# Performance work log

Hardware: AMD Instinct MI355X
Metric: run time of the kernel (lower is better)

The kernel has to match this reference:

```python
import jax, jax.numpy as jnp
import numpy as np

N = 100000   # nodes
E = 300000   # edges per snapshot
S = 5        # snapshots
D_IN = 128   # node_dim
H = 256      # hidden dim
P = 10000    # post nodes


def setup_inputs() -> dict:
    key = jax.random.key(0)
    ks = jax.random.split(key, 8)
    node_features = jax.random.normal(ks[0], (N, D_IN), jnp.float32)
    edge_index = jax.random.randint(ks[1], (S, 2, E), 0, N, dtype=jnp.int64)
    post_idx = jax.random.randint(ks[2], (P,), 0, N, dtype=jnp.int64)
    glorot = lambda k, sh, fan: jax.random.normal(k, sh, jnp.float32) * (1.0 / np.sqrt(fan))
    return {
        'node_features': node_features,
        'edge_index': edge_index,
        'post_idx': post_idx,
        'W1': glorot(ks[3], (D_IN, H), D_IN), 'b1': jnp.zeros((H,), jnp.float32),
        'W2': glorot(ks[4], (H, H), H),       'b2': jnp.zeros((H,), jnp.float32),
        'Wc1': glorot(ks[5], (H, H // 2), H), 'bc1': jnp.zeros((H // 2,), jnp.float32),
        'Wc2': glorot(ks[6], (H // 2, 1), H // 2), 'bc2': jnp.zeros((1,), jnp.float32),
    }


def gcn_conv(x, src, dst, W, b):
    """PyG GCNConv: h = D^-1/2 (A+I) D^-1/2 (x W) + b, aggregate at target (dst)."""
    n = x.shape[0]
    h = x @ W                                   # [n, out]
    loop = jnp.arange(n, dtype=src.dtype)
    src2 = jnp.concatenate([src, loop])          # add self-loops
    dst2 = jnp.concatenate([dst, loop])
    deg = jax.ops.segment_sum(jnp.ones_like(dst2, jnp.float32), dst2, num_segments=n)
    dinv = jnp.where(deg > 0, jax.lax.rsqrt(deg), 0.0)
    norm = dinv[src2] * dinv[dst2]               # [E+n]
    out = jax.ops.segment_sum(h[src2] * norm[:, None], dst2, num_segments=n)
    return out + b


def reference(node_features, edge_index, post_idx, W1, b1, W2, b2, Wc1, bc1, Wc2, bc2):
    embs = []
    for s in range(edge_index.shape[0]):  # loop over fixed small snapshot count
        src, dst = edge_index[s, 0], edge_index[s, 1]
        # layer 0: 128 -> 256, relu, no skip (dims differ)
        x1 = jax.nn.relu(gcn_conv(node_features, src, dst, W1, b1))
        # layer 1 (last): 256 -> 256, no relu, residual skip
        x2 = gcn_conv(x1, src, dst, W2, b2) + x1
        embs.append(x2)
    agg = jnp.mean(jnp.stack(embs, axis=0), axis=0)  # mean over snapshots
    post = agg[post_idx]                             # [P, H]
    logits = jax.nn.relu(post @ Wc1 + bc1) @ Wc2 + bc2
    return jax.nn.sigmoid(logits[:, 0])              # [P]
```

## Files before the change

kernel.cpp:

```cpp
#include <hip/hip_runtime.h>
#include <hip/hip_bf16.h>
#include <math.h>

#define NN 100000
#define NE 300000
#define NS 5
#define DIN 128
#define HID 256
#define NP 10000
#define NB_N 391

#define NBUCK 1024
#define NBUCK_USED 782
#define PBLK 64
#define EPB 19
#define BCAP 2048
#define CAPR 40960
#define NCPAD 16
#define LDB 136
#define LDO 260

typedef short s8v __attribute__((ext_vector_type(8)));
typedef float f4v __attribute__((ext_vector_type(4)));

static __device__ __forceinline__ float bf2f(unsigned short u) {
    union { unsigned int i; float f; } v; v.i = ((unsigned int)u) << 16; return v.f;
}
static __device__ __forceinline__ unsigned short f2bf(float f) {
    union { float f; unsigned int i; } v; v.f = f;
    return (unsigned short)((v.i + 0x7fff + ((v.i >> 16) & 1)) >> 16);
}


__global__ void setpost_kernel(const int* __restrict__ post, int* __restrict__ isPost,
                               int* __restrict__ needed) {
    int i = blockIdx.x * 256 + threadIdx.x;
    int s = blockIdx.y;
    if (i < NP) {
        int nd = post[i];
        needed[(size_t)s * NN + nd] = 1;
        if (s == 0) isPost[nd] = 1;
    }
}


__global__ void hist_kernel(const int* __restrict__ EI, int* __restrict__ bhist) {
    __shared__ int h[NBUCK];
    int s = blockIdx.y, b = blockIdx.x, t = threadIdx.x;
    for (int q = t; q < NBUCK; q += 256) h[q] = 0;
    __syncthreads();
    const int* dstp = EI + (size_t)s * 2 * NE + NE;
    int e0 = b * (EPB * 256);
    #pragma unroll
    for (int j = 0; j < EPB; j++) {
        int e = e0 + j * 256 + t;
        if (e < NE) atomicAdd(&h[dstp[e] >> 7], 1);
    }
    __syncthreads();
    for (int q = t; q < NBUCK; q += 256)
        if (h[q]) atomicAdd(&bhist[s * NBUCK + q], h[q]);
}

__global__ void bscan_kernel(const int* __restrict__ bhist, int* __restrict__ bbase,
                             int* __restrict__ bcur) {
    __shared__ int sm[NBUCK];
    int s = blockIdx.x, t = threadIdx.x;
    int v = bhist[s * NBUCK + t];
    sm[t] = v;
    __syncthreads();
    for (int d = 1; d < NBUCK; d <<= 1) {
        int x = (t >= d) ? sm[t - d] : 0;
        __syncthreads();
        sm[t] += x;
        __syncthreads();
    }
    int base = sm[t] - v;
    bbase[s * NBUCK + t] = base;
    bcur[s * NBUCK + t] = base;
}

__global__ void part_kernel(const int* __restrict__ EI, int* __restrict__ bcur,
                            int2* __restrict__ pairs) {
    __shared__ int h[NBUCK];
    __shared__ int base[NBUCK];
    int s = blockIdx.y, b = blockIdx.x, t = threadIdx.x;
    for (int q = t; q < NBUCK; q += 256) h[q] = 0;
    __syncthreads();
    const int* srcp = EI + (size_t)s * 2 * NE;
    const int* dstp = srcp + NE;
    int e0 = b * (EPB * 256);
    int rs[EPB], rd[EPB];
    #pragma unroll
    for (int j = 0; j < EPB; j++) {
        int e = e0 + j * 256 + t;
        if (e < NE) {
            rs[j] = srcp[e];
            rd[j] = dstp[e];
            atomicAdd(&h[rd[j] >> 7], 1);
        } else {
            rd[j] = -1; rs[j] = 0;
        }
    }
    __syncthreads();
    for (int q = t; q < NBUCK; q += 256) {
        int c = h[q];
        base[q] = c ? atomicAdd(&bcur[s * NBUCK + q], c) : 0;
    }
    __syncthreads();
    #pragma unroll
    for (int j = 0; j < EPB; j++) {
        if (rd[j] >= 0) {
            int pos = atomicAdd(&base[rd[j] >> 7], 1);
            pairs[(size_t)s * NE + pos] = make_int2(rs[j], rd[j]);
        }
    }
}

__global__ void bucket_csr_kernel(const int2* __restrict__ pairs, const int* __restrict__ bbase,
                                  const int* __restrict__ bhist, const int* __restrict__ isPost,
                                  int* __restrict__ cnt, int* __restrict__ offs,
                                  float* __restrict__ dinv, int* __restrict__ csr,
                                  int* __restrict__ needed) {
    __shared__ int nh[128];
    __shared__ int noff[128];
    __shared__ int sbuf[BCAP];
    int s = blockIdx.y, b = blockIdx.x, t = threadIdx.x;
    int base = bbase[s * NBUCK + b];
    int count = bhist[s * NBUCK + b];
    if (count > BCAP) count = BCAP;
    if (t < 128) nh[t] = 0;
    __syncthreads();
    const int2* pp = pairs + (size_t)s * NE + base;
    for (int e = t; e < count; e += 256)
        atomicAdd(&nh[pp[e].y & 127], 1);
    __syncthreads();
    if (t < 128) noff[t] = nh[t];
    __syncthreads();
    for (int d = 1; d < 128; d <<= 1) {
        int x = 0;
        if (t < 128 && t >= d) x = noff[t - d];
        __syncthreads();
        if (t < 128) noff[t] += x;
        __syncthreads();
    }
    if (t < 128) {
        int excl = noff[t] - nh[t];
        noff[t] = excl;
        int g = b * 128 + t;
        if (g < NN) {
            int c = nh[t];
            cnt[(size_t)s * NN + g]  = c;
            offs[(size_t)s * NN + g] = base + excl;
            dinv[(size_t)s * NN + g] = rsqrtf((float)(c + 1));
        }
    }
    __syncthreads();
    for (int e = t; e < count; e += 256) {
        int2 pr = pp[e];
        int pos = atomicAdd(&noff[pr.y & 127], 1);
        sbuf[pos] = pr.x;
        if (isPost[pr.y]) needed[(size_t)s * NN + pr.x] = 1;
    }
    __syncthreads();
    for (int e = t; e < count; e += 256)
        csr[(size_t)s * NE + base + e] = sbuf[e];
}


__global__ void compact_kernel(const int* __restrict__ needed, int* __restrict__ ncount,
                               int* __restrict__ list, int* __restrict__ inv) {
    __shared__ int wcnt[4];
    __shared__ int gbase;
    int s = blockIdx.y;
    int i = blockIdx.x * 256 + threadIdx.x;
    int wave = threadIdx.x >> 6, lane = threadIdx.x & 63;
    bool pred = (i < NN) && (needed[(size_t)s * NN + i] != 0);
    unsigned long long mask = __ballot(pred);
    int wc = __popcll(mask);
    if (lane == 0) wcnt[wave] = wc;
    __syncthreads();
    if (threadIdx.x == 0) {
        int tot = wcnt[0] + wcnt[1] + wcnt[2] + wcnt[3];
        gbase = tot ? atomicAdd(&ncount[s * NCPAD], tot) : 0;
    }
    __syncthreads();
    if (pred) {
        int wbase = gbase;
        #pragma unroll
        for (int q = 0; q < 4; q++) if (q < wave) wbase += wcnt[q];
        int rank = __popcll(mask & ((1ull << lane) - 1ull));
        int slot = wbase + rank;
        if (slot < CAPR) {
            list[(size_t)s * NN + slot] = i;
            inv[(size_t)s * NN + i] = slot;
        }
    }
}


__global__ void cvt_kernel(const float* __restrict__ src, unsigned short* __restrict__ dstp, int n4) {
    int i = blockIdx.x * 256 + threadIdx.x;
    if (i < n4) {
        float4 v = *(const float4*)&src[(size_t)i * 4];
        ushort4 o;
        o.x = f2bf(v.x); o.y = f2bf(v.y); o.z = f2bf(v.z); o.w = f2bf(v.w);
        *(ushort4*)&dstp[(size_t)i * 4] = o;
    }
}

__global__ void tw_kernel(const float* __restrict__ W, unsigned short* __restrict__ Wt,
                          int K, int Ncols) {
    int i = blockIdx.x * 256 + threadIdx.x;
    if (i < K * Ncols) {
        int n = i / K, k = i - n * K;
        Wt[i] = f2bf(W[(size_t)k * Ncols + n]);
    }
}


__global__ __launch_bounds__(512) void agg_mm1_kernel(
        const unsigned short* __restrict__ Xb, const unsigned short* __restrict__ W1t,
        const int* __restrict__ ncount, const float* __restrict__ dinvA,
        const int* __restrict__ offsA, const int* __restrict__ cntA,
        const int* __restrict__ csrA, const int* __restrict__ listA,
        const float* __restrict__ b1, unsigned short* __restrict__ x1cA) {
    int s = blockIdx.y;
    int M = ncount[s * NCPAD];
    if (M > CAPR) M = CAPR;
    if (blockIdx.x * 128 >= M) return;
    const float* dinv = dinvA + (size_t)s * NN;
    const int* offs = offsA + (size_t)s * NN;
    const int* cnt  = cntA + (size_t)s * NN;
    const int* csr  = csrA + (size_t)s * NE;
    const int* list = listA + (size_t)s * NN;
    unsigned short* x1c = x1cA + (size_t)s * CAPR * HID;

    __shared__ unsigned short ldsbuf[256 * LDB];
    int tid = threadIdx.x;
    for (int q = tid; q < 256 * 16; q += 512) {
        int n = q >> 4;
        int k8 = (q & 15) * 8;
        *(s8v*)&ldsbuf[n * LDB + k8] = *(const s8v*)&W1t[n * 128 + k8];
    }
    __syncthreads();

    int wave = tid >> 6, lane = tid & 63, lr = lane & 15, g = lane >> 4;
    int rowbase = blockIdx.x * 128 + wave * 16;
    int arow = rowbase + lr;

    float ga[4][8];
    #pragma unroll
    for (int kk = 0; kk < 4; kk++)
        #pragma unroll
        for (int j = 0; j < 8; j++) ga[kk][j] = 0.f;
    float di = 0.f;

    if (arow < M) {
        int node = list[arow];
        int o = offs[node], c = cnt[node];
        di = dinv[node];
        const unsigned short* rp = Xb + (size_t)node * DIN + g * 8;
        #pragma unroll
        for (int kk = 0; kk < 4; kk++) {
            s8v h = *(const s8v*)(rp + kk * 32);
            #pragma unroll
            for (int j = 0; j < 8; j++) ga[kk][j] = di * bf2f((unsigned short)h[j]);
        }
        for (int k = 0; k < c; k++) {
            int sv = csr[o + k];
            float wgt = dinv[sv];
            const unsigned short* sp = Xb + (size_t)sv * DIN + g * 8;
            #pragma unroll
            for (int kk = 0; kk < 4; kk++) {
                s8v h = *(const s8v*)(sp + kk * 32);
                #pragma unroll
                for (int j = 0; j < 8; j++) ga[kk][j] += wgt * bf2f((unsigned short)h[j]);
            }
        }
    }

    f4v acc[16];
    #pragma unroll
    for (int t8 = 0; t8 < 16; t8++) acc[t8] = (f4v){0.f, 0.f, 0.f, 0.f};
    #pragma unroll
    for (int kk = 0; kk < 4; kk++) {
        s8v a;
        #pragma unroll
        for (int j = 0; j < 8; j++) a[j] = (short)f2bf(ga[kk][j]);
        #pragma unroll
        for (int t8 = 0; t8 < 16; t8++) {
            s8v b = *(const s8v*)&ldsbuf[(t8 * 16 + lr) * LDB + kk * 32 + g * 8];
            acc[t8] = __builtin_amdgcn_mfma_f32_16x16x32_bf16(a, b, acc[t8], 0, 0, 0);
        }
    }

    __syncthreads();

    #pragma unroll
    for (int r = 0; r < 4; r++) {
        int lrow = wave * 16 + g * 4 + r;
        float sc = __shfl(di, g * 4 + r, 64);
        #pragma unroll
        for (int t8 = 0; t8 < 16; t8++) {
            int col = t8 * 16 + lr;
            float v = sc * acc[t8][r] + b1[col];
            ldsbuf[lrow * LDO + col] = f2bf(v > 0.f ? v : 0.f);
        }
    }
    __syncthreads();

    int nrows = M - blockIdx.x * 128;
    if (nrows > 128) nrows = 128;
    for (int q = tid; q < 128 * 32; q += 512) {
        int row = q >> 5;
        if (row < nrows) {
            int c8 = (q & 31) * 8;
            *(s8v*)&x1c[(size_t)(blockIdx.x * 128 + row) * HID + c8] =
                *(const s8v*)&ldsbuf[row * LDO + c8];
        }
    }
}


__global__ void z2_kernel(const unsigned short* __restrict__ x1cA, const float* __restrict__ dinvA,
                          const int* __restrict__ offsA, const int* __restrict__ cntA,
                          const int* __restrict__ csrA, const int* __restrict__ invA,
                          const int* __restrict__ post, unsigned short* __restrict__ z2bA) {
    int s = blockIdx.y;
    const unsigned short* x1c = x1cA + (size_t)s * CAPR * HID;
    const float* dinv = dinvA + (size_t)s * NN;
    const int* offs = offsA + (size_t)s * NN;
    const int* cnt  = cntA + (size_t)s * NN;
    const int* csr  = csrA + (size_t)s * NE;
    const int* inv  = invA + (size_t)s * NN;
    unsigned short* z2b = z2bA + (size_t)s * NP * HID;

    int wave = threadIdx.x >> 6, lane = threadIdx.x & 63;
    int eg = lane >> 4, el = lane & 15;
    int p = blockIdx.x * 4 + wave;
    if (p >= NP) return;
    int node = post[p];
    int o = offs[node], c = cnt[node];
    float acc0[8] = {0.f, 0.f, 0.f, 0.f, 0.f, 0.f, 0.f, 0.f};
    float acc1[8] = {0.f, 0.f, 0.f, 0.f, 0.f, 0.f, 0.f, 0.f};
    for (int k = eg; k < c; k += 4) {
        int sv = csr[o + k];
        float wgt = dinv[sv];
        int r = inv[sv];
        const unsigned short* rp = &x1c[(size_t)r * HID + el * 16];
        s8v h0 = *(const s8v*)rp;
        s8v h1 = *(const s8v*)(rp + 8);
        #pragma unroll
        for (int j = 0; j < 8; j++) {
            acc0[j] += wgt * bf2f((unsigned short)h0[j]);
            acc1[j] += wgt * bf2f((unsigned short)h1[j]);
        }
    }
    if (eg == 0) {
        float di = dinv[node];
        int r = inv[node];
        const unsigned short* rp = &x1c[(size_t)r * HID + el * 16];
        s8v h0 = *(const s8v*)rp;
        s8v h1 = *(const s8v*)(rp + 8);
        #pragma unroll
        for (int j = 0; j < 8; j++) {
            acc0[j] += di * bf2f((unsigned short)h0[j]);
            acc1[j] += di * bf2f((unsigned short)h1[j]);
        }
    }
    #pragma unroll
    for (int j = 0; j < 8; j++) {
        acc0[j] += __shfl_xor(acc0[j], 16, 64);
        acc0[j] += __shfl_xor(acc0[j], 32, 64);
        acc1[j] += __shfl_xor(acc1[j], 16, 64);
        acc1[j] += __shfl_xor(acc1[j], 32, 64);
    }
    if (eg == 0) {
        s8v o0, o1;
        #pragma unroll
        for (int j = 0; j < 8; j++) {
            o0[j] = (short)f2bf(acc0[j]);
            o1[j] = (short)f2bf(acc1[j]);
        }
        unsigned short* wp = &z2b[(size_t)p * HID + el * 16];
        *(s8v*)wp = o0;
        *(s8v*)(wp + 8) = o1;
    }
}


__global__ __launch_bounds__(512) void mm2_kernel(
        const unsigned short* __restrict__ z2bA,
        const unsigned short* __restrict__ W2t,
        const float* __restrict__ dinvA,
        const int* __restrict__ post,
        const int* __restrict__ invA,
        const float* __restrict__ b2,
        const unsigned short* __restrict__ x1cA,
        float* __restrict__ aggPA) {
    int s = blockIdx.z;
    const unsigned short* A = z2bA + (size_t)s * NP * HID;
    const float* dinv = dinvA + (size_t)s * NN;
    const int* inv = invA + (size_t)s * NN;
    const unsigned short* x1c = x1cA + (size_t)s * CAPR * HID;
    float* Out = aggPA + (size_t)s * NP * HID;

    __shared__ unsigned short lds[128 * (HID + 8)];
    int tid = threadIdx.x;
    int colbase = blockIdx.y * 128;
    for (int q = tid; q < 128 * 32; q += 512) {
        int n = q >> 5;
        int k8 = (q & 31) * 8;
        *(s8v*)&lds[n * (HID + 8) + k8] = *(const s8v*)&W2t[(size_t)(colbase + n) * HID + k8];
    }
    __syncthreads();

    int wave = tid >> 6, lane = tid & 63, lr = lane & 15, g = lane >> 4;
    int rowbase = blockIdx.x * 128 + wave * 16;
    int arow = rowbase + lr;

    f4v acc[8];
    #pragma unroll
    for (int t = 0; t < 8; t++) acc[t] = (f4v){0.f, 0.f, 0.f, 0.f};

    #pragma unroll
    for (int kk = 0; kk < HID / 32; kk++) {
        s8v a = (s8v){0, 0, 0, 0, 0, 0, 0, 0};
        if (arow < NP) a = *(const s8v*)&A[(size_t)arow * HID + kk * 32 + g * 8];
        #pragma unroll
        for (int t = 0; t < 8; t++) {
            s8v b = *(const s8v*)&lds[(t * 16 + lr) * (HID + 8) + kk * 32 + g * 8];
            acc[t] = __builtin_amdgcn_mfma_f32_16x16x32_bf16(a, b, acc[t], 0, 0, 0);
        }
    }

    int orow0 = rowbase + g * 4;
    #pragma unroll
    for (int r = 0; r < 4; r++) {
        int row = orow0 + r;
        if (row < NP) {
            int nd = post[row];
            float sc = dinv[nd];
            size_t x1row = (size_t)inv[nd] * HID;
            #pragma unroll
            for (int t = 0; t < 8; t++) {
                int col = colbase + t * 16 + lr;
                Out[(size_t)row * HID + col] =
                    sc * acc[t][r] + b2[col] + bf2f(x1c[x1row + col]);
            }
        }
    }
}


__global__ void redcvt_kernel(const float* __restrict__ aggPA, unsigned short* __restrict__ aggPb) {
    int i = blockIdx.x * 256 + threadIdx.x;
    if (i < NP * HID / 4) {
        float4 a = *(const float4*)&aggPA[(size_t)i * 4];
        #pragma unroll
        for (int s = 1; s < NS; s++) {
            float4 b = *(const float4*)&aggPA[(size_t)s * NP * HID + (size_t)i * 4];
            a.x += b.x; a.y += b.y; a.z += b.z; a.w += b.w;
        }
        ushort4 o;
        o.x = f2bf(a.x); o.y = f2bf(a.y); o.z = f2bf(a.z); o.w = f2bf(a.w);
        *(ushort4*)&aggPb[(size_t)i * 4] = o;
    }
}


__global__ void mm3_kernel(const unsigned short* __restrict__ A,
                           const unsigned short* __restrict__ Bt,
                           const float* __restrict__ bias,
                           float* __restrict__ Out) {
    int tid = threadIdx.x;
    int wave = tid >> 6, lane = tid & 63, lr = lane & 15, g = lane >> 4;
    int rowbase = blockIdx.x * 64 + wave * 16;
    int arow = rowbase + lr;

    f4v acc[8];
    #pragma unroll
    for (int t = 0; t < 8; t++) acc[t] = (f4v){0.f, 0.f, 0.f, 0.f};

    #pragma unroll
    for (int kk = 0; kk < HID / 32; kk++) {
        s8v a = (s8v){0, 0, 0, 0, 0, 0, 0, 0};
        if (arow < NP) a = *(const s8v*)&A[(size_t)arow * HID + kk * 32 + g * 8];
        #pragma unroll
        for (int t = 0; t < 8; t++) {
            s8v b = *(const s8v*)&Bt[(size_t)(t * 16 + lr) * HID + kk * 32 + g * 8];
            acc[t] = __builtin_amdgcn_mfma_f32_16x16x32_bf16(a, b, acc[t], 0, 0, 0);
        }
    }

    int orow0 = rowbase + g * 4;
    #pragma unroll
    for (int r = 0; r < 4; r++) {
        int row = orow0 + r;
        if (row < NP) {
            #pragma unroll
            for (int t = 0; t < 8; t++) {
                int col = t * 16 + lr;
                float v = 0.2f * acc[t][r] + bias[col];
                Out[(size_t)row * 128 + col] = v > 0.f ? v : 0.f;
            }
        }
    }
}

__global__ void final_kernel(const float* __restrict__ hid, const float* __restrict__ Wc2,
                             const float* __restrict__ bc2, float* __restrict__ out) {
    int wave = threadIdx.x >> 6;
    int lane = threadIdx.x & 63;
    int p = blockIdx.x * 4 + wave;
    if (p >= NP) return;
    float part = hid[(size_t)p * 128 + lane] * Wc2[lane]
               + hid[(size_t)p * 128 + 64 + lane] * Wc2[64 + lane];
    for (int off = 32; off; off >>= 1) part += __shfl_down(part, off, 64);
    if (lane == 0) out[p] = 1.f / (1.f + expf(-(part + bc2[0])));
}


extern "C" void kernel_launch(void* const* d_in, const int* in_sizes, int n_in,
                              void* d_out, int out_size, void* d_ws, size_t ws_size,
                              hipStream_t stream) {
    const float* X    = (const float*)d_in[0];
    const int*   EI   = (const int*)d_in[1];
    const int*   post = (const int*)d_in[2];
    const float* W1   = (const float*)d_in[3];
    const float* b1   = (const float*)d_in[4];
    const float* W2   = (const float*)d_in[5];
    const float* b2   = (const float*)d_in[6];
    const float* Wc1  = (const float*)d_in[7];
    const float* bc1  = (const float*)d_in[8];
    const float* Wc2  = (const float*)d_in[9];
    const float* bc2  = (const float*)d_in[10];
    float* out = (float*)d_out;

    char* w = (char*)d_ws;
    auto carve = [&](size_t bytes) {
        void* p = (void*)w;
        w += (bytes + 255) & ~(size_t)255;
        return p;
    };
    unsigned short* Xb    = (unsigned short*)carve((size_t)NN * DIN * 2);
    unsigned short* x1c   = (unsigned short*)carve((size_t)NS * CAPR * HID * 2);
    unsigned short* z2b5  = (unsigned short*)carve((size_t)NS * NP * HID * 2);
    float* aggP5          = (float*)carve((size_t)NS * NP * HID * 4);
    unsigned short* aggPb = (unsigned short*)carve((size_t)NP * HID * 2);
    float* hid            = (float*)carve((size_t)NP * 128 * 4);
    unsigned short* W1t   = (unsigned short*)carve((size_t)256 * 128 * 2);
    unsigned short* W2t   = (unsigned short*)carve((size_t)256 * 256 * 2);
    unsigned short* Wc1t  = (unsigned short*)carve((size_t)128 * 256 * 2);
    float* dinv           = (float*)carve((size_t)NS * NN * 4);
    int*   cnt            = (int*)carve((size_t)NS * NN * 4);
    int*   offs           = (int*)carve((size_t)NS * NN * 4);
    int*   needed         = (int*)carve((size_t)NS * NN * 4);
    int*   list           = (int*)carve((size_t)NS * NN * 4);
    int*   inv            = (int*)carve((size_t)NS * NN * 4);
    int*   isPost         = (int*)carve((size_t)NN * 4);
    int*   bhist          = (int*)carve((size_t)NS * NBUCK * 4);
    int*   bbase          = (int*)carve((size_t)NS * NBUCK * 4);
    int*   bcur           = (int*)carve((size_t)NS * NBUCK * 4);
    int*   ncount         = (int*)carve((size_t)NS * NCPAD * 4);
    int*   csr            = (int*)carve((size_t)NS * NE * 4);
    int2*  pairs          = (int2*)x1c;

    hipMemsetAsync(needed, 0, (size_t)NS * NN * 4, stream);
    hipMemsetAsync(isPost, 0, (size_t)NN * 4, stream);
    hipMemsetAsync(bhist, 0, (size_t)NS * NBUCK * 4, stream);
    hipMemsetAsync(ncount, 0, (size_t)NS * NCPAD * 4, stream);

    cvt_kernel<<<(NN * DIN / 4 + 255) / 256, 256, 0, stream>>>(X, Xb, NN * DIN / 4);
    tw_kernel<<<(128 * 256 + 255) / 256, 256, 0, stream>>>(W1, W1t, 128, 256);
    tw_kernel<<<(256 * 256 + 255) / 256, 256, 0, stream>>>(W2, W2t, 256, 256);
    tw_kernel<<<(256 * 128 + 255) / 256, 256, 0, stream>>>(Wc1, Wc1t, 256, 128);
    setpost_kernel<<<dim3((NP + 255) / 256, NS), 256, 0, stream>>>(post, isPost, needed);

    hist_kernel<<<dim3(PBLK, NS), 256, 0, stream>>>(EI, bhist);
    bscan_kernel<<<NS, NBUCK, 0, stream>>>(bhist, bbase, bcur);
    part_kernel<<<dim3(PBLK, NS), 256, 0, stream>>>(EI, bcur, pairs);
    bucket_csr_kernel<<<dim3(NBUCK_USED, NS), 256, 0, stream>>>(pairs, bbase, bhist, isPost,
                                                                cnt, offs, dinv, csr, needed);
    compact_kernel<<<dim3(NB_N, NS), 256, 0, stream>>>(needed, ncount, list, inv);

    agg_mm1_kernel<<<dim3((CAPR + 127) / 128, NS), 512, 0, stream>>>(
        Xb, W1t, ncount, dinv, offs, cnt, csr, list, b1, x1c);
    z2_kernel<<<dim3((NP + 3) / 4, NS), 256, 0, stream>>>(
        x1c, dinv, offs, cnt, csr, inv, post, z2b5);
    mm2_kernel<<<dim3((NP + 127) / 128, 2, NS), 512, 0, stream>>>(
        z2b5, W2t, dinv, post, inv, b2, x1c, aggP5);

    redcvt_kernel<<<(NP * HID / 4 + 255) / 256, 256, 0, stream>>>(aggP5, aggPb);
    mm3_kernel<<<(NP + 63) / 64, 256, 0, stream>>>(aggPb, Wc1t, bc1, hid);
    final_kernel<<<(NP + 3) / 4, 256, 0, stream>>>(hid, Wc2, bc2, out);
}
```

Baseline: 244.8 us.

## Fuse snapshot reduction into mm2, fuse classifier head, merge prep kernels

mm2 now loops over all five snapshots inside one block and accumulates the epilogue in registers, writing the bf16 snapshot-sum directly. This removes the fp32 per-snapshot aggP buffer and the separate redcvt pass. mm3 and the final dot/sigmoid are fused through an LDS tile, and the four weight/feature conversion kernels are merged into one launch. The trade-off is a smaller mm2 grid with each block doing five times the work, which cuts parallelism.

```diff
diff --git a/kernel.cpp b/kernel.cpp
--- a/kernel.cpp
+++ b/kernel.cpp
@@ -40,6 +40,33 @@
         int nd = post[i];
         needed[(size_t)s * NN + nd] = 1;
         if (s == 0) isPost[nd] = 1;
+    }
+}
+
+
+__global__ void prep_kernel(const float* __restrict__ X, unsigned short* __restrict__ Xb,
+                            const float* __restrict__ W1, unsigned short* __restrict__ W1t,
+                            const float* __restrict__ W2, unsigned short* __restrict__ W2t,
+                            const float* __restrict__ Wc1, unsigned short* __restrict__ Wc1t) {
+    int b = blockIdx.x, t = threadIdx.x;
+    if (b < 12500) {
+        int i = b * 256 + t;
+        float4 v = *(const float4*)&X[(size_t)i * 4];
+        ushort4 o;
+        o.x = f2bf(v.x); o.y = f2bf(v.y); o.z = f2bf(v.z); o.w = f2bf(v.w);
+        *(ushort4*)&Xb[(size_t)i * 4] = o;
+    } else if (b < 12628) {
+        int i = (b - 12500) * 256 + t;
+        int n = i >> 7, k = i & 127;
+        W1t[i] = f2bf(W1[(size_t)k * 256 + n]);
+    } else if (b < 12884) {
+        int i = (b - 12628) * 256 + t;
+        int n = i >> 8, k = i & 255;
+        W2t[i] = f2bf(W2[(size_t)k * 256 + n]);
+    } else {
+        int i = (b - 12884) * 256 + t;
+        int n = i >> 8, k = i & 255;
+        Wc1t[i] = f2bf(Wc1[(size_t)k * 128 + n]);
     }
 }
 
@@ -194,26 +221,6 @@
             list[(size_t)s * NN + slot] = i;
             inv[(size_t)s * NN + i] = slot;
         }
-    }
-}
-
-
-__global__ void cvt_kernel(const float* __restrict__ src, unsigned short* __restrict__ dstp, int n4) {
-    int i = blockIdx.x * 256 + threadIdx.x;
-    if (i < n4) {
-        float4 v = *(const float4*)&src[(size_t)i * 4];
-        ushort4 o;
-        o.x = f2bf(v.x); o.y = f2bf(v.y); o.z = f2bf(v.z); o.w = f2bf(v.w);
-        *(ushort4*)&dstp[(size_t)i * 4] = o;
-    }
-}
-
-__global__ void tw_kernel(const float* __restrict__ W, unsigned short* __restrict__ Wt,
-                          int K, int Ncols) {
-    int i = blockIdx.x * 256 + threadIdx.x;
-    if (i < K * Ncols) {
-        int n = i / K, k = i - n * K;
-        Wt[i] = f2bf(W[(size_t)k * Ncols + n]);
     }
 }
 
@@ -389,7 +396,7 @@
 }
 
 
-__global__ __launch_bounds__(512) void mm2_kernel(
+__global__ __launch_bounds__(256) void mm2_kernel(
         const unsigned short* __restrict__ z2bA,
         const unsigned short* __restrict__ W2t,
         const float* __restrict__ dinvA,
@@ -397,18 +404,11 @@
         const int* __restrict__ invA,
         const float* __restrict__ b2,
         const unsigned short* __restrict__ x1cA,
-        float* __restrict__ aggPA) {
-    int s = blockIdx.z;
-    const unsigned short* A = z2bA + (size_t)s * NP * HID;
-    const float* dinv = dinvA + (size_t)s * NN;
-    const int* inv = invA + (size_t)s * NN;
-    const unsigned short* x1c = x1cA + (size_t)s * CAPR * HID;
-    float* Out = aggPA + (size_t)s * NP * HID;
-
+        unsigned short* __restrict__ aggPb) {
     __shared__ unsigned short lds[128 * (HID + 8)];
     int tid = threadIdx.x;
     int colbase = blockIdx.y * 128;
-    for (int q = tid; q < 128 * 32; q += 512) {
+    for (int q = tid; q < 128 * 32; q += 256) {
         int n = q >> 5;
         int k8 = (q & 31) * 8;
         *(s8v*)&lds[n * (HID + 8) + k8] = *(const s8v*)&W2t[(size_t)(colbase + n) * HID + k8];
@@ -416,108 +416,113 @@
     __syncthreads();
 
     int wave = tid >> 6, lane = tid & 63, lr = lane & 15, g = lane >> 4;
-    int rowbase = blockIdx.x * 128 + wave * 16;
+    int rowbase = blockIdx.x * 64 + wave * 16;
     int arow = rowbase + lr;
-
-    f4v acc[8];
-    #pragma unroll
-    for (int t = 0; t < 8; t++) acc[t] = (f4v){0.f, 0.f, 0.f, 0.f};
-
-    #pragma unroll
-    for (int kk = 0; kk < HID / 32; kk++) {
-        s8v a = (s8v){0, 0, 0, 0, 0, 0, 0, 0};
-        if (arow < NP) a = *(const s8v*)&A[(size_t)arow * HID + kk * 32 + g * 8];
-        #pragma unroll
-        for (int t = 0; t < 8; t++) {
-            s8v b = *(const s8v*)&lds[(t * 16 + lr) * (HID + 8) + kk * 32 + g * 8];
-            acc[t] = __builtin_amdgcn_mfma_f32_16x16x32_bf16(a, b, acc[t], 0, 0, 0);
-        }
-    }
-
     int orow0 = rowbase + g * 4;
-    #pragma unroll
-    for (int r = 0; r < 4; r++) {
-        int row = orow0 + r;
-        if (row < NP) {
-            int nd = post[row];
-            float sc = dinv[nd];
-            size_t x1row = (size_t)inv[nd] * HID;
+
+    f4v epi[8];
+    #pragma unroll
+    for (int t = 0; t < 8; t++) epi[t] = (f4v){0.f, 0.f, 0.f, 0.f};
+
+    for (int s = 0; s < NS; s++) {
+        const unsigned short* A = z2bA + (size_t)s * NP * HID;
+        const float* dinv = dinvA + (size_t)s * NN;
+        const int* inv = invA + (size_t)s * NN;
+        const unsigned short* x1c = x1cA + (size_t)s * CAPR * HID;
+
+        f4v acc[8];
+        #pragma unroll
+        for (int t = 0; t < 8; t++) acc[t] = (f4v){0.f, 0.f, 0.f, 0.f};
+        #pragma unroll
+        for (int kk = 0; kk < HID / 32; kk++) {
+            s8v a = (s8v){0, 0, 0, 0, 0, 0, 0, 0};
+            if (arow < NP) a = *(const s8v*)&A[(size_t)arow * HID + kk * 32 + g * 8];
             #pragma unroll
             for (int t = 0; t < 8; t++) {
-                int col = colbase + t * 16 + lr;
-                Out[(size_t)row * HID + col] =
-                    sc * acc[t][r] + b2[col] + bf2f(x1c[x1row + col]);
+                s8v b = *(const s8v*)&lds[(t * 16 + lr) * (HID + 8) + kk * 32 + g * 8];
+                acc[t] = __builtin_amdgcn_mfma_f32_16x16x32_bf16(a, b, acc[t], 0, 0, 0);
             }
         }
-    }
-}
-
-
-__global__ void redcvt_kernel(const float* __restrict__ aggPA, unsigned short* __restrict__ aggPb) {
-    int i = blockIdx.x * 256 + threadIdx.x;
-    if (i < NP * HID / 4) {
-        float4 a = *(const float4*)&aggPA[(size_t)i * 4];
-        #pragma unroll
-        for (int s = 1; s < NS; s++) {
-            float4 b = *(const float4*)&aggPA[(size_t)s * NP * HID + (size_t)i * 4];
-            a.x += b.x; a.y += b.y; a.z += b.z; a.w += b.w;
-        }
-        ushort4 o;
-        o.x = f2bf(a.x); o.y = f2bf(a.y); o.z = f2bf(a.z); o.w = f2bf(a.w);
-        *(ushort4*)&aggPb[(size_t)i * 4] = o;
-    }
-}
-
-
-__global__ void mm3_kernel(const unsigned short* __restrict__ A,
-                           const unsigned short* __restrict__ Bt,
-                           const float* __restrict__ bias,
-                           float* __restrict__ Out) {
-    int tid = threadIdx.x;
-    int wave = tid >> 6, lane = tid & 63, lr = lane & 15, g = lane >> 4;
-    int rowbase = blockIdx.x * 64 + wave * 16;
-    int arow = rowbase + lr;
-
-    f4v acc[8];
-    #pragma unroll
-    for (int t = 0; t < 8; t++) acc[t] = (f4v){0.f, 0.f, 0.f, 0.f};
-
-    #pragma unroll
-    for (int kk = 0; kk < HID / 32; kk++) {
-        s8v a = (s8v){0, 0, 0, 0, 0, 0, 0, 0};
-        if (arow < NP) a = *(const s8v*)&A[(size_t)arow * HID + kk * 32 + g * 8];
-        #pragma unroll
-        for (int t = 0; t < 8; t++) {
-            s8v b = *(const s8v*)&Bt[(size_t)(t * 16 + lr) * HID + kk * 32 + g * 8];
-            acc[t] = __builtin_amdgcn_mfma_f32_16x16x32_bf16(a, b, acc[t], 0, 0, 0);
-        }
-    }
-
-    int orow0 = rowbase + g * 4;
+        #pragma unroll
+        for (int r = 0; r < 4; r++) {
+            int row = orow0 + r;
+            if (row < NP) {
+                int nd = post[row];
+                float sc = dinv[nd];
+                size_t x1row = (size_t)inv[nd] * HID;
+                #pragma unroll
+                for (int t = 0; t < 8; t++) {
+                    int col = colbase + t * 16 + lr;
+                    epi[t][r] += sc * acc[t][r] + bf2f(x1c[x1row + col]);
+                }
+            }
+        }
+    }
+
     #pragma unroll
     for (int r = 0; r < 4; r++) {
         int row = orow0 + r;
         if (row < NP) {
             #pragma unroll
             for (int t = 0; t < 8; t++) {
-                int col = t * 16 + lr;
-                float v = 0.2f * acc[t][r] + bias[col];
-                Out[(size_t)row * 128 + col] = v > 0.f ? v : 0.f;
+                int col = colbase + t * 16 + lr;
+                aggPb[(size_t)row * HID + col] = f2bf(epi[t][r] + (float)NS * b2[col]);
             }
         }
     }
 }
 
-__global__ void final_kernel(const float* __restrict__ hid, const float* __restrict__ Wc2,
-                             const float* __restrict__ bc2, float* __restrict__ out) {
-    int wave = threadIdx.x >> 6;
-    int lane = threadIdx.x & 63;
-    int p = blockIdx.x * 4 + wave;
-    if (p >= NP) return;
-    float part = hid[(size_t)p * 128 + lane] * Wc2[lane]
-               + hid[(size_t)p * 128 + 64 + lane] * Wc2[64 + lane];
-    for (int off = 32; off; off >>= 1) part += __shfl_down(part, off, 64);
-    if (lane == 0) out[p] = 1.f / (1.f + expf(-(part + bc2[0])));
+
+__global__ __launch_bounds__(256) void mm3f_kernel(
+        const unsigned short* __restrict__ A, const unsigned short* __restrict__ Bt,
+        const float* __restrict__ bc1, const float* __restrict__ Wc2,
+        const float* __restrict__ bc2, float* __restrict__ out) {
+    __shared__ float tile[64 * 133];
+    __shared__ float wc2s[128];
+    int tid = threadIdx.x;
+    if (tid < 128) wc2s[tid] = Wc2[tid];
+    int wave = tid >> 6, lane = tid & 63, lr = lane & 15, g = lane >> 4;
+    int rowbase = blockIdx.x * 64 + wave * 16;
+    int arow = rowbase + lr;
+
+    f4v acc[8];
+    #pragma unroll
+    for (int t = 0; t < 8; t++) acc[t] = (f4v){0.f, 0.f, 0.f, 0.f};
+
+    #pragma unroll
+    for (int kk = 0; kk < HID / 32; kk++) {
+        s8v a = (s8v){0, 0, 0, 0, 0, 0, 0, 0};
+        if (arow < NP) a = *(const s8v*)&A[(size_t)arow * HID + kk * 32 + g * 8];
+        #pragma unroll
+        for (int t = 0; t < 8; t++) {
+            s8v b = *(const s8v*)&Bt[(size_t)(t * 16 + lr) * HID + kk * 32 + g * 8];
+            acc[t] = __builtin_amdgcn_mfma_f32_16x16x32_bf16(a, b, acc[t], 0, 0, 0);
+        }
+    }
+
+    #pragma unroll
+    for (int r = 0; r < 4; r++) {
+        int lrow = wave * 16 + g * 4 + r;
+        #pragma unroll
+        for (int t = 0; t < 8; t++) {
+            int col = t * 16 + lr;
+            float v = 0.2f * acc[t][r] + bc1[col];
+            tile[lrow * 133 + col] = v > 0.f ? v : 0.f;
+        }
+    }
+    __syncthreads();
+
+    int lrow = wave * 16 + (lane >> 2);
+    int chunk = lane & 3;
+    float ssum = 0.f;
+    #pragma unroll
+    for (int j = 0; j < 32; j++)
+        ssum += tile[lrow * 133 + chunk + 4 * j] * wc2s[chunk + 4 * j];
+    ssum += __shfl_xor(ssum, 1, 64);
+    ssum += __shfl_xor(ssum, 2, 64);
+    int p = blockIdx.x * 64 + lrow;
+    if (chunk == 0 && p < NP)
+        out[p] = 1.f / (1.f + expf(-(ssum + bc2[0])));
 }
 
 
@@ -546,9 +551,7 @@
     unsigned short* Xb    = (unsigned short*)carve((size_t)NN * DIN * 2);
     unsigned short* x1c   = (unsigned short*)carve((size_t)NS * CAPR * HID * 2);
     unsigned short* z2b5  = (unsigned short*)carve((size_t)NS * NP * HID * 2);
-    float* aggP5          = (float*)carve((size_t)NS * NP * HID * 4);
     unsigned short* aggPb = (unsigned short*)carve((size_t)NP * HID * 2);
-    float* hid            = (float*)carve((size_t)NP * 128 * 4);
     unsigned short* W1t   = (unsigned short*)carve((size_t)256 * 128 * 2);
     unsigned short* W2t   = (unsigned short*)carve((size_t)256 * 256 * 2);
     unsigned short* Wc1t  = (unsigned short*)carve((size_t)128 * 256 * 2);
@@ -571,10 +574,7 @@
     hipMemsetAsync(bhist, 0, (size_t)NS * NBUCK * 4, stream);
     hipMemsetAsync(ncount, 0, (size_t)NS * NCPAD * 4, stream);
 
-    cvt_kernel<<<(NN * DIN / 4 + 255) / 256, 256, 0, stream>>>(X, Xb, NN * DIN / 4);
-    tw_kernel<<<(128 * 256 + 255) / 256, 256, 0, stream>>>(W1, W1t, 128, 256);
-    tw_kernel<<<(256 * 256 + 255) / 256, 256, 0, stream>>>(W2, W2t, 256, 256);
-    tw_kernel<<<(256 * 128 + 255) / 256, 256, 0, stream>>>(Wc1, Wc1t, 256, 128);
+    prep_kernel<<<13012, 256, 0, stream>>>(X, Xb, W1, W1t, W2, W2t, Wc1, Wc1t);
     setpost_kernel<<<dim3((NP + 255) / 256, NS), 256, 0, stream>>>(post, isPost, needed);
 
     hist_kernel<<<dim3(PBLK, NS), 256, 0, stream>>>(EI, bhist);
@@ -588,10 +588,8 @@
         Xb, W1t, ncount, dinv, offs, cnt, csr, list, b1, x1c);
     z2_kernel<<<dim3((NP + 3) / 4, NS), 256, 0, stream>>>(
         x1c, dinv, offs, cnt, csr, inv, post, z2b5);
-    mm2_kernel<<<dim3((NP + 127) / 128, 2, NS), 512, 0, stream>>>(
-        z2b5, W2t, dinv, post, inv, b2, x1c, aggP5);
-
-    redcvt_kernel<<<(NP * HID / 4 + 255) / 256, 256, 0, stream>>>(aggP5, aggPb);
-    mm3_kernel<<<(NP + 63) / 64, 256, 0, stream>>>(aggPb, Wc1t, bc1, hid);
-    final_kernel<<<(NP + 3) / 4, 256, 0, stream>>>(hid, Wc2, bc2, out);
-}
+    mm2_kernel<<<dim3((NP + 63) / 64, 2), 256, 0, stream>>>(
+        z2b5, W2t, dinv, post, inv, b2, x1c, aggPb);
+
+    mm3f_kernel<<<(NP + 63) / 64, 256, 0, stream>>>(aggPb, Wc1t, bc1, Wc2, bc2, out);
+}
```

Result: slower. 297.8 us (+21.6%).
